# Kernel tuning notes

Measured on AMD Instinct MI355X. Metric: run time of the kernel, lower is better.

The kernel has to match this reference:

```python
import jax, jax.numpy as jnp
import numpy as np

NUM_BINS = 64  # num_bins_target == num_bins_source (defaults)
C_WIN = 1.0    # c_target == c_source (defaults)
EPS_LOG = 1e-12


def _normalise(x):
    # normalise_torch(x, 0.0, 1.0): global min-max rescale to [0, 1]
    x = x.astype(jnp.float32)
    return (x - x.min()) / (x.max() - x.min())


def _cubic_bspline(x):
    # Parzen cubic B-spline window (support |x| < 2)
    ax = jnp.abs(x)
    inner = (4.0 - 6.0 * ax * ax + 3.0 * ax * ax * ax) / 6.0
    outer = (2.0 - ax) ** 3 / 6.0
    return jnp.where(ax < 1.0, inner, jnp.where(ax < 2.0, outer, 0.0))


def setup_inputs() -> dict:
    key = jax.random.key(0)
    k1, k2 = jax.random.split(key)
    target = jax.random.uniform(k1, (2, 1, 96, 96, 96), dtype=jnp.float32)
    source = jax.random.uniform(k2, (2, 1, 96, 96, 96), dtype=jnp.float32)
    return {"target": target, "source": source}


def reference(target, source):
    # pre-processing: normalise to [0,1], flatten spatial dims -> (B, 1, N)
    t = _normalise(target).reshape(target.shape[0], target.shape[1], -1)
    s = _normalise(source).reshape(source.shape[0], source.shape[1], -1)

    # histogram bins (after normalisation max-min == 1)
    bw_t = (t.max() - t.min()) / NUM_BINS
    bw_s = (s.max() - s.min()) / NUM_BINS
    bins_t = jnp.arange(NUM_BINS, dtype=jnp.float32)[:, None] * bw_t  # (bins, 1)
    bins_s = jnp.arange(NUM_BINS, dtype=jnp.float32)[:, None] * bw_s
    eps_t = C_WIN * bw_t
    eps_s = C_WIN * bw_s

    # broadcast: (bins,1) - (B,1,N) -> (B, bins, N)
    W_t = _cubic_bspline((bins_t - t) / eps_t)
    W_s = _cubic_bspline((bins_s - s) / eps_s)

    # joint histogram: (B, bins_t, bins_s)
    hist_joint = jnp.einsum('bin,bjn->bij', W_t, W_s) / (eps_t * eps_s)

    # distributions (normalised over the WHOLE tensor, incl. batch, as in torch)
    p_joint = hist_joint / hist_joint.sum()
    p_t = p_joint.sum(axis=2)  # (B, bins_t)
    p_s = p_joint.sum(axis=1)  # (B, bins_s)

    # entropies per batch element
    H_t = -jnp.sum(p_t * jnp.log(p_t + EPS_LOG), axis=1)
    H_s = -jnp.sum(p_s * jnp.log(p_s + EPS_LOG), axis=1)
    H_j = -jnp.sum(p_joint * jnp.log(p_joint + EPS_LOG), axis=(1, 2))

    # NMI loss (nmi=True default)
    return -jnp.mean((H_t + H_s) / H_j)
```

## Files before the change

### kernel.cpp

```cpp
#include <hip/hip_runtime.h>
#include <math.h>

#define BATCH_N 884736
#define NTOT   1769472
#define NCHUNKW 18
#define GBLK 384
#define GWAVES 768
#define KBLK 512
#define QS 190.0f

#define BBLK_B 1024
#define TILE_B 6144
#define WAVE_B 12288
#define MROW 66

#define OFF_GHIST 256
#define OFF_KBLK 36864

typedef int v4i __attribute__((ext_vector_type(4)));
typedef int v2i __attribute__((ext_vector_type(2)));

__device__ __forceinline__ unsigned fkey(float x){
    unsigned u = __float_as_uint(x);
    return (u & 0x80000000u) ? ~u : (u | 0x80000000u);
}
__device__ __forceinline__ float fdecode(unsigned k){
    return __uint_as_float((k & 0x80000000u) ? (k ^ 0x80000000u) : ~k);
}

__device__ __forceinline__ void bw4(float u, float w[4]){
    float um = 1.f - u;
    float u2 = u*u, um2 = um*um;
    w[0] = um2*um*(1.f/6.f);
    w[3] = u2*u*(1.f/6.f);
    w[1] = 0.6666666666666667f - u2 + 0.5f*u2*u;
    w[2] = 0.6666666666666667f - um2 + 0.5f*um2*um;
}

__global__ void __launch_bounds__(256)
k_minmax(const float4* __restrict__ t4, const float4* __restrict__ s4,
         int n4, uint4* __restrict__ kblk, float* __restrict__ ghist){
    __shared__ unsigned red[4][4];

    if (blockIdx.x < 8){
        ghist[blockIdx.x*1024 + threadIdx.x] = 0.f;
        ghist[blockIdx.x*1024 + 256 + threadIdx.x] = 0.f;
        ghist[blockIdx.x*1024 + 512 + threadIdx.x] = 0.f;
        ghist[blockIdx.x*1024 + 768 + threadIdx.x] = 0.f;
    }

    unsigned mt=0u, mnt=0u, ms=0u, mns=0u;
    int stride = gridDim.x * blockDim.x;
    for (int i = blockIdx.x*blockDim.x + threadIdx.x; i < n4; i += stride){
        float4 a = t4[i];
        float4 b = s4[i];
        mt  = max(mt,  max(max(fkey(a.x),  fkey(a.y)),  max(fkey(a.z),  fkey(a.w))));
        mnt = max(mnt, max(max(fkey(-a.x), fkey(-a.y)), max(fkey(-a.z), fkey(-a.w))));
        ms  = max(ms,  max(max(fkey(b.x),  fkey(b.y)),  max(fkey(b.z),  fkey(b.w))));
        mns = max(mns, max(max(fkey(-b.x), fkey(-b.y)), max(fkey(-b.z), fkey(-b.w))));
    }
    #pragma unroll
    for (int off = 32; off; off >>= 1){
        mt  = max(mt,  __shfl_down(mt,  off));
        mnt = max(mnt, __shfl_down(mnt, off));
        ms  = max(ms,  __shfl_down(ms,  off));
        mns = max(mns, __shfl_down(mns, off));
    }
    int wid = threadIdx.x >> 6;
    if ((threadIdx.x & 63) == 0){
        red[wid][0] = mt; red[wid][1] = mnt; red[wid][2] = ms; red[wid][3] = mns;
    }
    __syncthreads();
    if (threadIdx.x == 0){
        uint4 q;
        q.x = max(max(red[0][0], red[1][0]), max(red[2][0], red[3][0]));
        q.y = max(max(red[0][1], red[1][1]), max(red[2][1], red[3][1]));
        q.z = max(max(red[0][2], red[1][2]), max(red[2][2], red[3][2]));
        q.w = max(max(red[0][3], red[1][3]), max(red[2][3], red[3][3]));
        kblk[blockIdx.x] = q;
    }
}

__global__ void __launch_bounds__(128, 3)
k_gemm(const float* __restrict__ t, const float* __restrict__ s,
       const uint4* __restrict__ kblk, float* __restrict__ ghist){
    __shared__ __align__(1024) int4 smem4[2*WAVE_B/16];
    __shared__ unsigned kred[2][4];

    int tid = threadIdx.x;
    int lane = tid & 63;
    int warp = tid >> 6;
    int rrow = lane & 15;
    int kgrp = lane >> 4;
    int b = blockIdx.y;

    char* As = (char*)smem4 + warp*WAVE_B;
    char* Bs = As + TILE_B;

    {
        int4* wz = (int4*)As;
        int4 z4 = {0,0,0,0};
        #pragma unroll
        for (int i = 0; i < 12; ++i)
            wz[i*64 + lane] = z4;
    }

    {
        unsigned m0=0u, m1=0u, m2=0u, m3=0u;
        #pragma unroll
        for (int i = 0; i < 4; ++i){
            uint4 q = kblk[tid + i*128];
            m0 = max(m0, q.x); m1 = max(m1, q.y);
            m2 = max(m2, q.z); m3 = max(m3, q.w);
        }
        #pragma unroll
        for (int off = 32; off; off >>= 1){
            m0 = max(m0, __shfl_down(m0, off));
            m1 = max(m1, __shfl_down(m1, off));
            m2 = max(m2, __shfl_down(m2, off));
            m3 = max(m3, __shfl_down(m3, off));
        }
        if (lane == 0){
            kred[warp][0] = m0; kred[warp][1] = m1;
            kred[warp][2] = m2; kred[warp][3] = m3;
        }
        __syncthreads();
    }
    float tmax =  fdecode(max(kred[0][0], kred[1][0]));
    float tmin = -fdecode(max(kred[0][1], kred[1][1]));
    float smax =  fdecode(max(kred[0][2], kred[1][2]));
    float smin = -fdecode(max(kred[0][3], kred[1][3]));
    float tsc = 64.f / (tmax - tmin);
    float ssc = 64.f / (smax - smin);

    const float* tb = t + (size_t)b*BATCH_N;
    const float* sb = s + (size_t)b*BATCH_N;

    v4i acc[4][4];
    #pragma unroll
    for (int i = 0; i < 4; ++i)
        #pragma unroll
        for (int j = 0; j < 4; ++j)
            acc[i][j] = (v4i){0,0,0,0};

    int c0 = blockIdx.x*2 + warp;
    int vrow = ((lane >> 3) << 7) + ((lane & 7) << 4);
    unsigned abase = (unsigned)(unsigned long long)As;
    unsigned bbase = (unsigned)(unsigned long long)Bs;

    float tq0 = tb[(size_t)c0*64 + lane];
    float sq0 = sb[(size_t)c0*64 + lane];
    float tq1 = tb[(size_t)(c0 + GWAVES)*64 + lane];
    float sq1 = sb[(size_t)(c0 + GWAVES)*64 + lane];

    for (int it = 0; it < NCHUNKW; ++it){
        int cpre = c0 + (it < NCHUNKW-2 ? (it + 2)*GWAVES : 0);
        float tnn = tb[(size_t)cpre*64 + lane];
        float snn = sb[(size_t)cpre*64 + lane];

        float vt = (tq0 - tmin) * tsc;
        int it0 = (int)vt;
        float wt[4]; bw4(vt - (float)it0, wt);
        unsigned Wa = (unsigned)__float2int_rn(wt[0]*QS)
                    | ((unsigned)__float2int_rn(wt[1]*QS) << 8)
                    | ((unsigned)__float2int_rn(wt[2]*QS) << 16)
                    | ((unsigned)__float2int_rn(wt[3]*QS) << 24);
        int ca = it0 + 15;
        int ga = ca >> 4, sha = (ca & 15) << 3;
        unsigned long long Wa64 = Wa;
        unsigned long long alo = (sha < 64) ? (Wa64 << sha) : 0ull;
        unsigned long long ahi = (sha < 64) ? (sha ? (Wa64 >> (64 - sha)) : 0ull)
                                            : (Wa64 << (sha - 64));
        unsigned long long asp = (sha > 96) ? (Wa64 >> (128 - sha)) : 0ull;

        float vs = (sq0 - smin) * ssc;
        int is0 = (int)vs;
        float wsv[4]; bw4(vs - (float)is0, wsv);
        unsigned Wb = (unsigned)__float2int_rn(wsv[0]*QS)
                    | ((unsigned)__float2int_rn(wsv[1]*QS) << 8)
                    | ((unsigned)__float2int_rn(wsv[2]*QS) << 16)
                    | ((unsigned)__float2int_rn(wsv[3]*QS) << 24);
        int cb = is0 + 15;
        int gb = cb >> 4, shb = (cb & 15) << 3;
        unsigned long long Wb64 = Wb;
        unsigned long long blo = (shb < 64) ? (Wb64 << shb) : 0ull;
        unsigned long long bhi = (shb < 64) ? (shb ? (Wb64 >> (64 - shb)) : 0ull)
                                            : (Wb64 << (shb - 64));
        unsigned long long bsp = (shb > 96) ? (Wb64 >> (128 - shb)) : 0ull;

        char* pa = As + ga*BBLK_B + vrow;
        char* pb = Bs + gb*BBLK_B + vrow;
        *(v4i*)pa            = (v4i){(int)alo, (int)(alo>>32), (int)ahi, (int)(ahi>>32)};
        *(v4i*)(pa + BBLK_B) = (v4i){(int)asp, (int)(asp>>32), 0, 0};
        *(v4i*)pb            = (v4i){(int)blo, (int)(blo>>32), (int)bhi, (int)(bhi>>32)};
        *(v4i*)(pb + BBLK_B) = (v4i){(int)bsp, (int)(bsp>>32), 0, 0};

        __asm__ volatile("" ::: "memory");

        v2i a00,a01,a10,a11,a20,a21,a30,a31;
        v2i b00,b01,b10,b11,b20,b21,b30,b31;
        asm volatile("ds_read_b64_tr_b8 %0, %1 offset:1024" : "=v"(a00) : "v"(abase));
        asm volatile("ds_read_b64_tr_b8 %0, %1 offset:1536" : "=v"(a01) : "v"(abase));
        asm volatile("ds_read_b64_tr_b8 %0, %1 offset:2048" : "=v"(a10) : "v"(abase));
        asm volatile("ds_read_b64_tr_b8 %0, %1 offset:2560" : "=v"(a11) : "v"(abase));
        asm volatile("ds_read_b64_tr_b8 %0, %1 offset:3072" : "=v"(a20) : "v"(abase));
        asm volatile("ds_read_b64_tr_b8 %0, %1 offset:3584" : "=v"(a21) : "v"(abase));
        asm volatile("ds_read_b64_tr_b8 %0, %1 offset:4096" : "=v"(a30) : "v"(abase));
        asm volatile("ds_read_b64_tr_b8 %0, %1 offset:4608" : "=v"(a31) : "v"(abase));
        asm volatile("ds_read_b64_tr_b8 %0, %1 offset:1024" : "=v"(b00) : "v"(bbase));
        asm volatile("ds_read_b64_tr_b8 %0, %1 offset:1536" : "=v"(b01) : "v"(bbase));
        asm volatile("ds_read_b64_tr_b8 %0, %1 offset:2048" : "=v"(b10) : "v"(bbase));
        asm volatile("ds_read_b64_tr_b8 %0, %1 offset:2560" : "=v"(b11) : "v"(bbase));
        asm volatile("ds_read_b64_tr_b8 %0, %1 offset:3072" : "=v"(b20) : "v"(bbase));
        asm volatile("ds_read_b64_tr_b8 %0, %1 offset:3584" : "=v"(b21) : "v"(bbase));
        asm volatile("ds_read_b64_tr_b8 %0, %1 offset:4096" : "=v"(b30) : "v"(bbase));
        asm volatile("ds_read_b64_tr_b8 %0, %1 offset:4608" : "=v"(b31) : "v"(bbase));
        asm volatile("s_waitcnt lgkmcnt(0)" ::: "memory");
        __builtin_amdgcn_sched_barrier(0);

        v4i af[4], bf[4];
        af[0] = (v4i){a00.x, a00.y, a01.x, a01.y};
        af[1] = (v4i){a10.x, a10.y, a11.x, a11.y};
        af[2] = (v4i){a20.x, a20.y, a21.x, a21.y};
        af[3] = (v4i){a30.x, a30.y, a31.x, a31.y};
        bf[0] = (v4i){b00.x, b00.y, b01.x, b01.y};
        bf[1] = (v4i){b10.x, b10.y, b11.x, b11.y};
        bf[2] = (v4i){b20.x, b20.y, b21.x, b21.y};
        bf[3] = (v4i){b30.x, b30.y, b31.x, b31.y};
        #pragma unroll
        for (int m = 0; m < 4; ++m)
            #pragma unroll
            for (int n = 0; n < 4; ++n)
                acc[m][n] = __builtin_amdgcn_mfma_i32_16x16x64_i8(af[m], bf[n], acc[m][n], 0, 0, 0);

        __asm__ volatile("" ::: "memory");
        {
            v4i z = (v4i){0,0,0,0};
            *(v4i*)pa = z; *(v4i*)(pa + BBLK_B) = z;
            *(v4i*)pb = z; *(v4i*)(pb + BBLK_B) = z;
        }

        tq0 = tq1; sq0 = sq1;
        tq1 = tnn; sq1 = snn;
    }

    const float dq = 1.f / (QS*QS);
    float* fm = (float*)smem4;
    __syncthreads();
    if (warp == 0){
        #pragma unroll
        for (int m = 0; m < 4; ++m)
            #pragma unroll
            for (int n = 0; n < 4; ++n)
                #pragma unroll
                for (int r = 0; r < 4; ++r)
                    fm[(m*16 + kgrp*4 + r)*MROW + n*16 + rrow] = (float)acc[m][n][r] * dq;
    }
    __syncthreads();
    if (warp == 1){
        #pragma unroll
        for (int m = 0; m < 4; ++m)
            #pragma unroll
            for (int n = 0; n < 4; ++n)
                #pragma unroll
                for (int r = 0; r < 4; ++r)
                    fm[(m*16 + kgrp*4 + r)*MROW + n*16 + rrow] += (float)acc[m][n][r] * dq;
    }
    __syncthreads();
    {
        float* g = ghist + b*4096;
        #pragma unroll
        for (int i = 0; i < 32; ++i){
            int idx = i*128 + tid;
            unsafeAtomicAdd(&g[idx], fm[(idx >> 6)*MROW + (idx & 63)]);
        }
    }
}

__device__ __forceinline__ float blockReduceSum(float v, float* red){
    #pragma unroll
    for (int off = 32; off; off >>= 1) v += __shfl_down(v, off);
    int wid = threadIdx.x >> 6, lane = threadIdx.x & 63;
    __syncthreads();
    if (lane == 0) red[wid] = v;
    __syncthreads();
    return red[0] + red[1] + red[2] + red[3];
}

__global__ void k_final(const float* __restrict__ hist, float* __restrict__ out){
    __shared__ float sh[2*4096];
    __shared__ float red[4];
    int tid = threadIdx.x;
    for (int i = tid; i < 8192; i += 256) sh[i] = hist[i];
    __syncthreads();

    float loc = 0.f;
    for (int i = tid; i < 8192; i += 256) loc += sh[i];
    float total = blockReduceSum(loc, red);
    float inv = 1.f / total;

    float nmi[2];
    for (int b = 0; b < 2; ++b){
        const float* h = sh + b*4096;
        float lj = 0.f;
        for (int i = tid; i < 4096; i += 256){
            float p = h[i]*inv;
            lj += p*logf(p + 1e-12f);
        }
        float Hj = -blockReduceSum(lj, red);
        float lt = 0.f;
        if (tid < 64){
            float r = 0.f;
            for (int j = 0; j < 64; ++j) r += h[tid*64 + j];
            float p = r*inv;
            lt = p*logf(p + 1e-12f);
        }
        float Ht = -blockReduceSum(lt, red);
        float ls = 0.f;
        if (tid < 64){
            float c = 0.f;
            for (int j = 0; j < 64; ++j) c += h[j*64 + tid];
            float p = c*inv;
            ls = p*logf(p + 1e-12f);
        }
        float Hs = -blockReduceSum(ls, red);
        nmi[b] = (Ht + Hs) / Hj;
    }
    if (tid == 0) out[0] = -0.5f*(nmi[0] + nmi[1]);
}

extern "C" void kernel_launch(void* const* d_in, const int* in_sizes, int n_in,
                              void* d_out, int out_size, void* d_ws, size_t ws_size,
                              hipStream_t stream) {
    const float* t = (const float*)d_in[0];
    const float* s = (const float*)d_in[1];
    float* out = (float*)d_out;
    float* ghist = (float*)((char*)d_ws + OFF_GHIST);
    uint4* kblk  = (uint4*)((char*)d_ws + OFF_KBLK);

    k_minmax<<<KBLK, 256, 0, stream>>>((const float4*)t, (const float4*)s, NTOT/4, kblk, ghist);
    k_gemm<<<dim3(GBLK, 2), 128, 0, stream>>>(t, s, kblk, ghist);
    k_final<<<1, 256, 0, stream>>>(ghist, out);
}
```

Measured before the change: 107.1 us.

## Use four waves per block and pipeline B-spline packing under LDS reads

The histogram GEMM kernel now runs four waves per block instead of two, which doubles the number of waves and halves the chunk iterations each wave processes. The B-spline weight packing for the next chunk is moved into the loop body after the transposed LDS reads are issued, so its ALU work can overlap the LDS latency. The per-block reduction now sums pairs of wave accumulators into two LDS slabs and adds them before the global atomics. This trades more LDS per block and more live registers for better latency hiding.

```diff
diff --git a/kernel.cpp b/kernel.cpp
--- a/kernel.cpp
+++ b/kernel.cpp
@@ -3,9 +3,11 @@
 
 #define BATCH_N 884736
 #define NTOT   1769472
-#define NCHUNKW 18
-#define GBLK 384
-#define GWAVES 768
+#define WPB 4
+#define THREADS 256
+#define GBX 384
+#define GWAVES 1536
+#define NCHUNK 9
 #define KBLK 512
 #define QS 190.0f
 
@@ -36,6 +38,26 @@
     w[1] = 0.6666666666666667f - u2 + 0.5f*u2*u;
     w[2] = 0.6666666666666667f - um2 + 0.5f*um2*um;
 }
+
+#define PACK(val, mn, sc, G, MV, SV) do { \
+    float v_ = ((val) - (mn)) * (sc); \
+    int i0_ = (int)v_; \
+    float w_[4]; bw4(v_ - (float)i0_, w_); \
+    unsigned W_ = (unsigned)__float2int_rn(w_[0]*QS) \
+                | ((unsigned)__float2int_rn(w_[1]*QS) << 8) \
+                | ((unsigned)__float2int_rn(w_[2]*QS) << 16) \
+                | ((unsigned)__float2int_rn(w_[3]*QS) << 24); \
+    int c_ = i0_ + 15; \
+    G = c_ >> 4; \
+    int sh_ = (c_ & 15) << 3; \
+    unsigned long long W64_ = W_; \
+    unsigned long long lo_ = (sh_ < 64) ? (W64_ << sh_) : 0ull; \
+    unsigned long long hi_ = (sh_ < 64) ? (sh_ ? (W64_ >> (64 - sh_)) : 0ull) \
+                                        : (W64_ << (sh_ - 64)); \
+    unsigned long long sp_ = (sh_ > 96) ? (W64_ >> (128 - sh_)) : 0ull; \
+    MV = (v4i){(int)lo_, (int)(lo_>>32), (int)hi_, (int)(hi_>>32)}; \
+    SV = (v4i){(int)sp_, (int)(sp_>>32), 0, 0}; \
+} while(0)
 
 __global__ void __launch_bounds__(256)
 k_minmax(const float4* __restrict__ t4, const float4* __restrict__ s4,
@@ -81,11 +103,11 @@
     }
 }
 
-__global__ void __launch_bounds__(128, 3)
+__global__ void __launch_bounds__(THREADS, 3)
 k_gemm(const float* __restrict__ t, const float* __restrict__ s,
        const uint4* __restrict__ kblk, float* __restrict__ ghist){
-    __shared__ __align__(1024) int4 smem4[2*WAVE_B/16];
-    __shared__ unsigned kred[2][4];
+    __shared__ __align__(1024) int4 smem4[WPB*WAVE_B/16];
+    __shared__ unsigned kred[WPB][4];
 
     int tid = threadIdx.x;
     int lane = tid & 63;
@@ -108,8 +130,8 @@
     {
         unsigned m0=0u, m1=0u, m2=0u, m3=0u;
         #pragma unroll
-        for (int i = 0; i < 4; ++i){
-            uint4 q = kblk[tid + i*128];
+        for (int i = 0; i < 2; ++i){
+            uint4 q = kblk[tid + i*256];
             m0 = max(m0, q.x); m1 = max(m1, q.y);
             m2 = max(m2, q.z); m3 = max(m3, q.w);
         }
@@ -126,10 +148,14 @@
         }
         __syncthreads();
     }
-    float tmax =  fdecode(max(kred[0][0], kred[1][0]));
-    float tmin = -fdecode(max(kred[0][1], kred[1][1]));
-    float smax =  fdecode(max(kred[0][2], kred[1][2]));
-    float smin = -fdecode(max(kred[0][3], kred[1][3]));
+    unsigned k0=0u,k1=0u,k2=0u,k3=0u;
+    #pragma unroll
+    for (int j = 0; j < WPB; ++j){
+        k0 = max(k0, kred[j][0]); k1 = max(k1, kred[j][1]);
+        k2 = max(k2, kred[j][2]); k3 = max(k3, kred[j][3]);
+    }
+    float tmax =  fdecode(k0), tmin = -fdecode(k1);
+    float smax =  fdecode(k2), smin = -fdecode(k3);
     float tsc = 64.f / (tmax - tmin);
     float ssc = 64.f / (smax - smin);
 
@@ -143,8 +169,8 @@
         for (int j = 0; j < 4; ++j)
             acc[i][j] = (v4i){0,0,0,0};
 
-    int c0 = blockIdx.x*2 + warp;
-    int vrow = ((lane >> 3) << 7) + ((lane & 7) << 4);
+    int c0 = blockIdx.x*WPB + warp;
+    int vrow = lane << 4;
     unsigned abase = (unsigned)(unsigned long long)As;
     unsigned bbase = (unsigned)(unsigned long long)Bs;
 
@@ -153,47 +179,17 @@
     float tq1 = tb[(size_t)(c0 + GWAVES)*64 + lane];
     float sq1 = sb[(size_t)(c0 + GWAVES)*64 + lane];
 
-    for (int it = 0; it < NCHUNKW; ++it){
-        int cpre = c0 + (it < NCHUNKW-2 ? (it + 2)*GWAVES : 0);
-        float tnn = tb[(size_t)cpre*64 + lane];
-        float snn = sb[(size_t)cpre*64 + lane];
-
-        float vt = (tq0 - tmin) * tsc;
-        int it0 = (int)vt;
-        float wt[4]; bw4(vt - (float)it0, wt);
-        unsigned Wa = (unsigned)__float2int_rn(wt[0]*QS)
-                    | ((unsigned)__float2int_rn(wt[1]*QS) << 8)
-                    | ((unsigned)__float2int_rn(wt[2]*QS) << 16)
-                    | ((unsigned)__float2int_rn(wt[3]*QS) << 24);
-        int ca = it0 + 15;
-        int ga = ca >> 4, sha = (ca & 15) << 3;
-        unsigned long long Wa64 = Wa;
-        unsigned long long alo = (sha < 64) ? (Wa64 << sha) : 0ull;
-        unsigned long long ahi = (sha < 64) ? (sha ? (Wa64 >> (64 - sha)) : 0ull)
-                                            : (Wa64 << (sha - 64));
-        unsigned long long asp = (sha > 96) ? (Wa64 >> (128 - sha)) : 0ull;
-
-        float vs = (sq0 - smin) * ssc;
-        int is0 = (int)vs;
-        float wsv[4]; bw4(vs - (float)is0, wsv);
-        unsigned Wb = (unsigned)__float2int_rn(wsv[0]*QS)
-                    | ((unsigned)__float2int_rn(wsv[1]*QS) << 8)
-                    | ((unsigned)__float2int_rn(wsv[2]*QS) << 16)
-                    | ((unsigned)__float2int_rn(wsv[3]*QS) << 24);
-        int cb = is0 + 15;
-        int gb = cb >> 4, shb = (cb & 15) << 3;
-        unsigned long long Wb64 = Wb;
-        unsigned long long blo = (shb < 64) ? (Wb64 << shb) : 0ull;
-        unsigned long long bhi = (shb < 64) ? (shb ? (Wb64 >> (64 - shb)) : 0ull)
-                                            : (Wb64 << (shb - 64));
-        unsigned long long bsp = (shb > 96) ? (Wb64 >> (128 - shb)) : 0ull;
-
+    v4i av0, av1, bv0, bv1; int ga, gb;
+    PACK(tq0, tmin, tsc, ga, av0, av1);
+    PACK(sq0, smin, ssc, gb, bv0, bv1);
+
+    for (int it = 0; it < NCHUNK; ++it){
         char* pa = As + ga*BBLK_B + vrow;
         char* pb = Bs + gb*BBLK_B + vrow;
-        *(v4i*)pa            = (v4i){(int)alo, (int)(alo>>32), (int)ahi, (int)(ahi>>32)};
-        *(v4i*)(pa + BBLK_B) = (v4i){(int)asp, (int)(asp>>32), 0, 0};
-        *(v4i*)pb            = (v4i){(int)blo, (int)(blo>>32), (int)bhi, (int)(bhi>>32)};
-        *(v4i*)(pb + BBLK_B) = (v4i){(int)bsp, (int)(bsp>>32), 0, 0};
+        *(v4i*)pa            = av0;
+        *(v4i*)(pa + BBLK_B) = av1;
+        *(v4i*)pb            = bv0;
+        *(v4i*)(pb + BBLK_B) = bv1;
 
         __asm__ volatile("" ::: "memory");
 
@@ -215,6 +211,14 @@
         asm volatile("ds_read_b64_tr_b8 %0, %1 offset:3584" : "=v"(b21) : "v"(bbase));
         asm volatile("ds_read_b64_tr_b8 %0, %1 offset:4096" : "=v"(b30) : "v"(bbase));
         asm volatile("ds_read_b64_tr_b8 %0, %1 offset:4608" : "=v"(b31) : "v"(bbase));
+
+        int cpre = c0 + (it < NCHUNK-2 ? (it + 2)*GWAVES : 0);
+        float tnn = tb[(size_t)cpre*64 + lane];
+        float snn = sb[(size_t)cpre*64 + lane];
+        v4i nav0, nav1, nbv0, nbv1; int nga, ngb;
+        PACK(tq1, tmin, tsc, nga, nav0, nav1);
+        PACK(sq1, smin, ssc, ngb, nbv0, nbv1);
+
         asm volatile("s_waitcnt lgkmcnt(0)" ::: "memory");
         __builtin_amdgcn_sched_barrier(0);
 
@@ -240,39 +244,44 @@
             *(v4i*)pb = z; *(v4i*)(pb + BBLK_B) = z;
         }
 
+        av0 = nav0; av1 = nav1; ga = nga;
+        bv0 = nbv0; bv1 = nbv1; gb = ngb;
         tq0 = tq1; sq0 = sq1;
         tq1 = tnn; sq1 = snn;
     }
 
     const float dq = 1.f / (QS*QS);
-    float* fm = (float*)smem4;
-    __syncthreads();
-    if (warp == 0){
+    float* fmw = (float*)((char*)smem4 + (warp >> 1)*(2*WAVE_B));
+    __syncthreads();
+    if ((warp & 1) == 0){
         #pragma unroll
         for (int m = 0; m < 4; ++m)
             #pragma unroll
             for (int n = 0; n < 4; ++n)
                 #pragma unroll
                 for (int r = 0; r < 4; ++r)
-                    fm[(m*16 + kgrp*4 + r)*MROW + n*16 + rrow] = (float)acc[m][n][r] * dq;
-    }
-    __syncthreads();
-    if (warp == 1){
+                    fmw[(m*16 + kgrp*4 + r)*MROW + n*16 + rrow] = (float)acc[m][n][r] * dq;
+    }
+    __syncthreads();
+    if ((warp & 1) == 1){
         #pragma unroll
         for (int m = 0; m < 4; ++m)
             #pragma unroll
             for (int n = 0; n < 4; ++n)
                 #pragma unroll
                 for (int r = 0; r < 4; ++r)
-                    fm[(m*16 + kgrp*4 + r)*MROW + n*16 + rrow] += (float)acc[m][n][r] * dq;
+                    fmw[(m*16 + kgrp*4 + r)*MROW + n*16 + rrow] += (float)acc[m][n][r] * dq;
     }
     __syncthreads();
     {
+        const float* fm0 = (const float*)smem4;
+        const float* fm1 = (const float*)((char*)smem4 + 2*WAVE_B);
         float* g = ghist + b*4096;
         #pragma unroll
-        for (int i = 0; i < 32; ++i){
-            int idx = i*128 + tid;
-            unsafeAtomicAdd(&g[idx], fm[(idx >> 6)*MROW + (idx & 63)]);
+        for (int i = 0; i < 16; ++i){
+            int idx = i*256 + tid;
+            int l = (idx >> 6)*MROW + (idx & 63);
+            unsafeAtomicAdd(&g[idx], fm0[l] + fm1[l]);
         }
     }
 }
@@ -339,6 +348,6 @@
     uint4* kblk  = (uint4*)((char*)d_ws + OFF_KBLK);
 
     k_minmax<<<KBLK, 256, 0, stream>>>((const float4*)t, (const float4*)s, NTOT/4, kblk, ghist);
-    k_gemm<<<dim3(GBLK, 2), 128, 0, stream>>>(t, s, kblk, ghist);
+    k_gemm<<<dim3(GBX, 2), THREADS, 0, stream>>>(t, s, kblk, ghist);
     k_final<<<1, 256, 0, stream>>>(ghist, out);
 }
```

Result: no change. 105.7 us (-1.3%).
